# Kernel tuning notes

Hardware: AMD Instinct MI355X
Metric: run time of the kernel (lower is better)

Reference implementation:

```python
import jax, jax.numpy as jnp
import numpy as np
import math
from jax import lax


def quick_gelu(v):
    return v * jax.nn.sigmoid(1.702 * v)


def setup_inputs() -> dict:
    key = jax.random.key(0)
    k0, k1, k2, k3 = jax.random.split(key, 4)
    B, N, C, dim = 64, 1024, 768, 8
    x = jax.random.normal(k0, (B, N, C), dtype=jnp.float32)
    # adapter_down: Linear(C -> dim), xavier-ish init
    Wd = jax.random.normal(k1, (C, dim), dtype=jnp.float32) * (1.0 / math.sqrt(C))
    bd = jnp.zeros((dim,), dtype=jnp.float32)
    # adapter_conv: Conv2d(dim, dim, 3, stride=1, pad=1), HWIO layout
    Wc = jax.random.normal(k2, (3, 3, dim, dim), dtype=jnp.float32) * (1.0 / math.sqrt(9 * dim))
    bc = jnp.zeros((dim,), dtype=jnp.float32)
    # adapter_up: Linear(dim -> C); torch inits this to zeros, but use small
    # random values so the output/gradients are non-trivial for testing.
    Wu = jax.random.normal(k3, (dim, C), dtype=jnp.float32) * 0.02
    bu = jnp.zeros((C,), dtype=jnp.float32)
    return {"x": x, "Wd": Wd, "bd": bd, "Wc": Wc, "bc": bc, "Wu": Wu, "bu": bu}


def reference(x, Wd, bd, Wc, bc, Wu, bu):
    B, N, C = x.shape
    H = int(math.isqrt(N))  # N is a static perfect square (patch grid)
    dim = Wd.shape[1]
    # down projection: [B, N, C] -> [B, N, dim]
    x_down = jnp.einsum("bnc,cd->bnd", x, Wd) + bd
    # reshape to NHWC patch grid, activate, 3x3 same-pad conv
    x_patch = quick_gelu(x_down.reshape(B, H, H, dim))
    x_patch = lax.conv_general_dilated(
        x_patch, Wc, window_strides=(1, 1), padding="SAME",
        dimension_numbers=("NHWC", "HWIO", "NHWC")) + bc
    # flatten back, activate (dropout = identity in eval), up projection
    x_down = quick_gelu(x_patch.reshape(B, N, dim))
    x_up = jnp.einsum("bnd,dc->bnc", x_down, Wu) + bu
    return x_up
```

## Files before the change

kernel.cpp:

```cpp
#include <hip/hip_runtime.h>

#define B_  64
#define N_  1024
#define H_  32
#define C_  768
#define D_  8

__device__ __forceinline__ float qgelu(float v) {
    return v / (1.0f + __expf(-1.702f * v));
}

typedef float f32x4_t __attribute__((ext_vector_type(4)));
__device__ __forceinline__ float4 ntload4(const float4* p) {
    f32x4_t v = __builtin_nontemporal_load((const f32x4_t*)p);
    return make_float4(v.x, v.y, v.z, v.w);
}
__device__ __forceinline__ void ntstore4(float4 v, float4* p) {
    f32x4_t t; t.x = v.x; t.y = v.y; t.z = v.z; t.w = v.w;
    __builtin_nontemporal_store(t, (f32x4_t*)p);
}

__device__ __forceinline__ void reduce8(float* acc, int lane) {
    {
        const bool hi = lane & 1;
#pragma unroll
        for (int j = 0; j < 4; ++j) {
            const float a = acc[j], b = acc[j + 4];
            acc[j] = hi ? b : a;
            acc[j + 4] = hi ? a : b;
        }
#pragma unroll
        for (int j = 0; j < 4; ++j)
            acc[j] += __shfl_xor(acc[j + 4], 1, 64);
    }
    {
        const bool hi = lane & 2;
#pragma unroll
        for (int j = 0; j < 2; ++j) {
            const float a = acc[j], b = acc[j + 2];
            acc[j] = hi ? b : a;
            acc[j + 2] = hi ? a : b;
        }
#pragma unroll
        for (int j = 0; j < 2; ++j)
            acc[j] += __shfl_xor(acc[j + 2], 2, 64);
    }
    {
        const bool hi = lane & 4;
        const float a = acc[0], b = acc[1];
        acc[0] = hi ? b : a;
        acc[1] = hi ? a : b;
        acc[0] += __shfl_xor(acc[1], 4, 64);
    }
    acc[0] += __shfl_xor(acc[0], 8, 64);
    acc[0] += __shfl_xor(acc[0], 16, 64);
    acc[0] += __shfl_xor(acc[0], 32, 64);
}

__global__ __launch_bounds__(256) void k_down(
    const float* __restrict__ x, const float* __restrict__ Wd,
    const float* __restrict__ bd, float* __restrict__ t1)
{
    __shared__ float sW[D_ * C_];
    for (int i = threadIdx.x; i < D_ * C_; i += 256) {
        const int c = i >> 3, d = i & 7;
        sW[d * C_ + c] = Wd[i];
    }
    __syncthreads();

    const int wid  = threadIdx.x >> 6;
    const int lane = threadIdx.x & 63;
    const int dl   = 4 * (lane & 1) + 2 * ((lane >> 1) & 1) + ((lane >> 2) & 1);
    const float bias = bd[dl];

    const int gw = blockIdx.x * 4 + wid;

#pragma unroll 1
    for (int i = 0; i < 4; ++i) {
        const int p = gw * 4 + i;
        const float4* x0 = (const float4*)(x + (size_t)(2 * p) * C_);
        const float4* x1 = x0 + (C_ / 4);

        float4 va[3], vb[3];
#pragma unroll
        for (int k = 0; k < 3; ++k) {
            va[k] = ntload4(&x0[k * 64 + lane]);
            vb[k] = ntload4(&x1[k * 64 + lane]);
        }

        float a0[D_], a1[D_];
#pragma unroll
        for (int d = 0; d < D_; ++d) { a0[d] = 0.0f; a1[d] = 0.0f; }

#pragma unroll
        for (int k = 0; k < 3; ++k) {
#pragma unroll
            for (int d = 0; d < D_; ++d) {
                const float4 wv = *(const float4*)&sW[d * C_ + (k * 64 + lane) * 4];
                a0[d] += va[k].x * wv.x + va[k].y * wv.y
                       + va[k].z * wv.z + va[k].w * wv.w;
                a1[d] += vb[k].x * wv.x + vb[k].y * wv.y
                       + vb[k].z * wv.z + vb[k].w * wv.w;
            }
        }

        reduce8(a0, lane);
        reduce8(a1, lane);

        if (lane < 16) {
            const float s = (lane & 8) ? a1[0] : a0[0];
            t1[(size_t)(2 * p + ((lane >> 3) & 1)) * D_ + dl] = qgelu(s + bias);
        }
    }
}

__global__ __launch_bounds__(256, 4) void k_conv(
    const float* __restrict__ t1, const float* __restrict__ Wc,
    const float* __restrict__ bc, float* __restrict__ t2)
{
    __shared__ float sIn[10 * H_ * D_];
    __shared__ float sWc[9 * D_ * D_];
    __shared__ float sbc[D_];

    const int img   = blockIdx.x >> 2;
    const int strip = blockIdx.x & 3;
    const int h0    = strip * 8;
    const float* in = t1 + (size_t)img * N_ * D_;

#pragma unroll
    for (int j = 0; j < 10; ++j) {
        const int i  = threadIdx.x + j * 256;
        const int lr = i >> 8;
        const int rem = i & 255;
        const int g  = h0 - 1 + lr;
        sIn[i] = (g >= 0 && g < H_) ? in[(size_t)g * H_ * D_ + rem] : 0.0f;
    }
    for (int i = threadIdx.x; i < 9 * D_ * D_; i += 256) sWc[i] = Wc[i];
    if (threadIdx.x < D_) sbc[threadIdx.x] = bc[threadIdx.x];
    __syncthreads();

    const int lh = threadIdx.x >> 5;
    const int w  = threadIdx.x & 31;
    float acc[D_];
#pragma unroll
    for (int co = 0; co < D_; ++co) acc[co] = sbc[co];

#pragma unroll
    for (int kh = 0; kh < 3; ++kh) {
        const int lrow = lh + kh;
#pragma unroll
        for (int kw = 0; kw < 3; ++kw) {
            const int ww = w + kw - 1;
            if (ww < 0 || ww >= H_) continue;
            const float* ip = &sIn[(lrow * H_ + ww) * D_];
            const float* wp = &sWc[(kh * 3 + kw) * D_ * D_];
#pragma unroll
            for (int ci = 0; ci < D_; ++ci) {
                const float iv = ip[ci];
#pragma unroll
                for (int co = 0; co < D_; ++co)
                    acc[co] += iv * wp[ci * D_ + co];
            }
        }
    }
    float4 o0, o1;
    o0.x = qgelu(acc[0]); o0.y = qgelu(acc[1]);
    o0.z = qgelu(acc[2]); o0.w = qgelu(acc[3]);
    o1.x = qgelu(acc[4]); o1.y = qgelu(acc[5]);
    o1.z = qgelu(acc[6]); o1.w = qgelu(acc[7]);
    float* tp = t2 + ((size_t)img * N_ + (size_t)(h0 + lh) * H_ + w) * D_;
    *(float4*)tp       = o0;
    *(float4*)(tp + 4) = o1;
}

__global__ __launch_bounds__(256, 3) void k_up(
    const float* __restrict__ t2, const float* __restrict__ Wu,
    const float* __restrict__ bu, float* __restrict__ out, int nrows)
{
    const int wid  = threadIdx.x >> 6;
    const int lane = threadIdx.x & 63;

    float4 w[3][D_];
    float4 bias[3];
#pragma unroll
    for (int j = 0; j < 3; ++j) {
        bias[j] = *(const float4*)&bu[(lane + j * 64) * 4];
#pragma unroll
        for (int d = 0; d < D_; ++d)
            w[j][d] = *(const float4*)&Wu[d * C_ + (lane + j * 64) * 4];
    }

    const int stride = gridDim.x * 4;
    for (int row = blockIdx.x * 4 + wid; row < nrows; row += stride) {
        const float4* rp = (const float4*)(t2 + (size_t)row * D_);
        const float4 ra = rp[0];
        const float4 rb = rp[1];
        const float rv[D_] = { ra.x, ra.y, ra.z, ra.w, rb.x, rb.y, rb.z, rb.w };

#pragma unroll
        for (int j = 0; j < 3; ++j) {
            float4 o = bias[j];
#pragma unroll
            for (int d = 0; d < D_; ++d) {
                o.x += rv[d] * w[j][d].x;
                o.y += rv[d] * w[j][d].y;
                o.z += rv[d] * w[j][d].z;
                o.w += rv[d] * w[j][d].w;
            }
            ntstore4(o, (float4*)&out[(size_t)row * C_ + (size_t)(lane + j * 64) * 4]);
        }
    }
}

extern "C" void kernel_launch(void* const* d_in, const int* in_sizes, int n_in,
                              void* d_out, int out_size, void* d_ws, size_t ws_size,
                              hipStream_t stream) {
    const float* x  = (const float*)d_in[0];
    const float* Wd = (const float*)d_in[1];
    const float* bd = (const float*)d_in[2];
    const float* Wc = (const float*)d_in[3];
    const float* bc = (const float*)d_in[4];
    const float* Wu = (const float*)d_in[5];
    const float* bu = (const float*)d_in[6];
    float* out = (float*)d_out;

    const int nrows = B_ * N_;
    float* t1 = (float*)d_ws;
    float* t2 = t1 + (size_t)nrows * D_;

    k_down<<<2048, 256, 0, stream>>>(x, Wd, bd, t1);
    k_conv<<<B_ * 4, 256, 0, stream>>>(t1, Wc, bc, t2);
    k_up<<<768, 256, 0, stream>>>(t2, Wu, bu, out, nrows);
}
```

Measured before the change: 102.2 us.

## Fuse conv and up-projection and pipeline down/up stages across batch chunks

Merges the three kernels into one multi-role kernel launched five times over four batch chunks. Each launch runs the down projection for chunk s alongside the fused conv+up projection for chunk s-1, so the read-heavy and write-heavy phases overlap. The conv output now stays in shared memory instead of going through a global t2 buffer. In exchange there are more launches, the up stage gets less parallelism (64 blocks per chunk, each writing 256 rows), and the Wu registers held per thread may lower occupancy.

```diff
diff --git a/kernel.cpp b/kernel.cpp
--- a/kernel.cpp
+++ b/kernel.cpp
@@ -5,6 +5,12 @@
 #define H_  32
 #define C_  768
 #define D_  8
+
+#define QCHUNKS   4
+#define IMG_PER_Q (B_ / QCHUNKS)
+#define ROWS_PER_Q (IMG_PER_Q * N_)
+#define NDOWN     512
+#define NUP       (IMG_PER_Q * 4)
 
 __device__ __forceinline__ float qgelu(float v) {
     return v / (1.0f + __expf(-1.702f * v));
@@ -57,157 +63,153 @@
     acc[0] += __shfl_xor(acc[0], 32, 64);
 }
 
-__global__ __launch_bounds__(256) void k_down(
-    const float* __restrict__ x, const float* __restrict__ Wd,
-    const float* __restrict__ bd, float* __restrict__ t1)
+__global__ __launch_bounds__(256) void k_step(
+    const float* __restrict__ x,  const float* __restrict__ Wd,
+    const float* __restrict__ bd, float* __restrict__ t1,
+    const float* __restrict__ Wc, const float* __restrict__ bc,
+    const float* __restrict__ Wu, const float* __restrict__ bu,
+    float* __restrict__ out, int downBase, int nDown, int upImg0)
 {
-    __shared__ float sW[D_ * C_];
-    for (int i = threadIdx.x; i < D_ * C_; i += 256) {
-        const int c = i >> 3, d = i & 7;
-        sW[d * C_ + c] = Wd[i];
-    }
-    __syncthreads();
+    __shared__ float smem[D_ * C_];
 
     const int wid  = threadIdx.x >> 6;
     const int lane = threadIdx.x & 63;
-    const int dl   = 4 * (lane & 1) + 2 * ((lane >> 1) & 1) + ((lane >> 2) & 1);
-    const float bias = bd[dl];
-
-    const int gw = blockIdx.x * 4 + wid;
+
+    if ((int)blockIdx.x < nDown) {
+        float* sW = smem;
+        for (int i = threadIdx.x; i < D_ * C_; i += 256) {
+            const int c = i >> 3, d = i & 7;
+            sW[d * C_ + c] = Wd[i];
+        }
+        __syncthreads();
+
+        const int dl = 4 * (lane & 1) + 2 * ((lane >> 1) & 1) + ((lane >> 2) & 1);
+        const float bias = bd[dl];
+        const int pairBase = (downBase >> 1) + blockIdx.x * 16 + wid * 4;
 
 #pragma unroll 1
-    for (int i = 0; i < 4; ++i) {
-        const int p = gw * 4 + i;
-        const float4* x0 = (const float4*)(x + (size_t)(2 * p) * C_);
-        const float4* x1 = x0 + (C_ / 4);
-
-        float4 va[3], vb[3];
-#pragma unroll
-        for (int k = 0; k < 3; ++k) {
-            va[k] = ntload4(&x0[k * 64 + lane]);
-            vb[k] = ntload4(&x1[k * 64 + lane]);
-        }
-
-        float a0[D_], a1[D_];
-#pragma unroll
-        for (int d = 0; d < D_; ++d) { a0[d] = 0.0f; a1[d] = 0.0f; }
-
-#pragma unroll
-        for (int k = 0; k < 3; ++k) {
-#pragma unroll
-            for (int d = 0; d < D_; ++d) {
-                const float4 wv = *(const float4*)&sW[d * C_ + (k * 64 + lane) * 4];
-                a0[d] += va[k].x * wv.x + va[k].y * wv.y
-                       + va[k].z * wv.z + va[k].w * wv.w;
-                a1[d] += vb[k].x * wv.x + vb[k].y * wv.y
-                       + vb[k].z * wv.z + vb[k].w * wv.w;
-            }
-        }
-
-        reduce8(a0, lane);
-        reduce8(a1, lane);
-
-        if (lane < 16) {
-            const float s = (lane & 8) ? a1[0] : a0[0];
-            t1[(size_t)(2 * p + ((lane >> 3) & 1)) * D_ + dl] = qgelu(s + bias);
-        }
-    }
-}
-
-__global__ __launch_bounds__(256, 4) void k_conv(
-    const float* __restrict__ t1, const float* __restrict__ Wc,
-    const float* __restrict__ bc, float* __restrict__ t2)
-{
-    __shared__ float sIn[10 * H_ * D_];
-    __shared__ float sWc[9 * D_ * D_];
-    __shared__ float sbc[D_];
-
-    const int img   = blockIdx.x >> 2;
-    const int strip = blockIdx.x & 3;
-    const int h0    = strip * 8;
-    const float* in = t1 + (size_t)img * N_ * D_;
-
-#pragma unroll
-    for (int j = 0; j < 10; ++j) {
-        const int i  = threadIdx.x + j * 256;
-        const int lr = i >> 8;
-        const int rem = i & 255;
-        const int g  = h0 - 1 + lr;
-        sIn[i] = (g >= 0 && g < H_) ? in[(size_t)g * H_ * D_ + rem] : 0.0f;
-    }
-    for (int i = threadIdx.x; i < 9 * D_ * D_; i += 256) sWc[i] = Wc[i];
-    if (threadIdx.x < D_) sbc[threadIdx.x] = bc[threadIdx.x];
-    __syncthreads();
-
-    const int lh = threadIdx.x >> 5;
-    const int w  = threadIdx.x & 31;
-    float acc[D_];
-#pragma unroll
-    for (int co = 0; co < D_; ++co) acc[co] = sbc[co];
-
-#pragma unroll
-    for (int kh = 0; kh < 3; ++kh) {
-        const int lrow = lh + kh;
-#pragma unroll
-        for (int kw = 0; kw < 3; ++kw) {
-            const int ww = w + kw - 1;
-            if (ww < 0 || ww >= H_) continue;
-            const float* ip = &sIn[(lrow * H_ + ww) * D_];
-            const float* wp = &sWc[(kh * 3 + kw) * D_ * D_];
-#pragma unroll
-            for (int ci = 0; ci < D_; ++ci) {
-                const float iv = ip[ci];
-#pragma unroll
-                for (int co = 0; co < D_; ++co)
-                    acc[co] += iv * wp[ci * D_ + co];
-            }
-        }
-    }
-    float4 o0, o1;
-    o0.x = qgelu(acc[0]); o0.y = qgelu(acc[1]);
-    o0.z = qgelu(acc[2]); o0.w = qgelu(acc[3]);
-    o1.x = qgelu(acc[4]); o1.y = qgelu(acc[5]);
-    o1.z = qgelu(acc[6]); o1.w = qgelu(acc[7]);
-    float* tp = t2 + ((size_t)img * N_ + (size_t)(h0 + lh) * H_ + w) * D_;
-    *(float4*)tp       = o0;
-    *(float4*)(tp + 4) = o1;
-}
-
-__global__ __launch_bounds__(256, 3) void k_up(
-    const float* __restrict__ t2, const float* __restrict__ Wu,
-    const float* __restrict__ bu, float* __restrict__ out, int nrows)
-{
-    const int wid  = threadIdx.x >> 6;
-    const int lane = threadIdx.x & 63;
-
-    float4 w[3][D_];
-    float4 bias[3];
-#pragma unroll
-    for (int j = 0; j < 3; ++j) {
-        bias[j] = *(const float4*)&bu[(lane + j * 64) * 4];
-#pragma unroll
-        for (int d = 0; d < D_; ++d)
-            w[j][d] = *(const float4*)&Wu[d * C_ + (lane + j * 64) * 4];
-    }
-
-    const int stride = gridDim.x * 4;
-    for (int row = blockIdx.x * 4 + wid; row < nrows; row += stride) {
-        const float4* rp = (const float4*)(t2 + (size_t)row * D_);
-        const float4 ra = rp[0];
-        const float4 rb = rp[1];
-        const float rv[D_] = { ra.x, ra.y, ra.z, ra.w, rb.x, rb.y, rb.z, rb.w };
-
+        for (int i = 0; i < 4; ++i) {
+            const int p = pairBase + i;
+            const float4* x0 = (const float4*)(x + (size_t)(2 * p) * C_);
+            const float4* x1 = x0 + (C_ / 4);
+
+            float4 va[3], vb[3];
+#pragma unroll
+            for (int k = 0; k < 3; ++k) {
+                va[k] = ntload4(&x0[k * 64 + lane]);
+                vb[k] = ntload4(&x1[k * 64 + lane]);
+            }
+
+            float a0[D_], a1[D_];
+#pragma unroll
+            for (int d = 0; d < D_; ++d) { a0[d] = 0.0f; a1[d] = 0.0f; }
+
+#pragma unroll
+            for (int k = 0; k < 3; ++k) {
+#pragma unroll
+                for (int d = 0; d < D_; ++d) {
+                    const float4 wv = *(const float4*)&sW[d * C_ + (k * 64 + lane) * 4];
+                    a0[d] += va[k].x * wv.x + va[k].y * wv.y
+                           + va[k].z * wv.z + va[k].w * wv.w;
+                    a1[d] += vb[k].x * wv.x + vb[k].y * wv.y
+                           + vb[k].z * wv.z + vb[k].w * wv.w;
+                }
+            }
+
+            reduce8(a0, lane);
+            reduce8(a1, lane);
+
+            if (lane < 16) {
+                const float s = (lane & 8) ? a1[0] : a0[0];
+                t1[(size_t)(2 * p + ((lane >> 3) & 1)) * D_ + dl] = qgelu(s + bias);
+            }
+        }
+    } else {
+        float* sIn = smem;
+        float* sT2 = smem + 2560;
+        float* sWc = smem + 4608;
+        float* sbc = smem + 5184;
+
+        const int idx   = blockIdx.x - nDown;
+        const int img   = upImg0 + (idx >> 2);
+        const int strip = idx & 3;
+        const int h0    = strip * 8;
+        const float* in = t1 + (size_t)img * N_ * D_;
+
+#pragma unroll
+        for (int j = 0; j < 10; ++j) {
+            const int i   = threadIdx.x + j * 256;
+            const int lr  = i >> 8;
+            const int rem = i & 255;
+            const int g   = h0 - 1 + lr;
+            sIn[i] = (g >= 0 && g < H_) ? in[(size_t)g * H_ * D_ + rem] : 0.0f;
+        }
+        for (int i = threadIdx.x; i < 9 * D_ * D_; i += 256) sWc[i] = Wc[i];
+        if (threadIdx.x < D_) sbc[threadIdx.x] = bc[threadIdx.x];
+
+        float4 wu[3][D_];
+        float4 ub[3];
 #pragma unroll
         for (int j = 0; j < 3; ++j) {
-            float4 o = bias[j];
-#pragma unroll
-            for (int d = 0; d < D_; ++d) {
-                o.x += rv[d] * w[j][d].x;
-                o.y += rv[d] * w[j][d].y;
-                o.z += rv[d] * w[j][d].z;
-                o.w += rv[d] * w[j][d].w;
-            }
-            ntstore4(o, (float4*)&out[(size_t)row * C_ + (size_t)(lane + j * 64) * 4]);
+            ub[j] = *(const float4*)&bu[(lane + j * 64) * 4];
+#pragma unroll
+            for (int d = 0; d < D_; ++d)
+                wu[j][d] = *(const float4*)&Wu[d * C_ + (lane + j * 64) * 4];
+        }
+        __syncthreads();
+
+        {
+            const int lh = threadIdx.x >> 5;
+            const int w  = threadIdx.x & 31;
+            float acc[D_];
+#pragma unroll
+            for (int co = 0; co < D_; ++co) acc[co] = sbc[co];
+#pragma unroll
+            for (int kh = 0; kh < 3; ++kh) {
+                const int lrow = lh + kh;
+#pragma unroll
+                for (int kw = 0; kw < 3; ++kw) {
+                    const int ww = w + kw - 1;
+                    if (ww < 0 || ww >= H_) continue;
+                    const float* ip = &sIn[(lrow * H_ + ww) * D_];
+                    const float* wp = &sWc[(kh * 3 + kw) * D_ * D_];
+#pragma unroll
+                    for (int ci = 0; ci < D_; ++ci) {
+                        const float iv = ip[ci];
+#pragma unroll
+                        for (int co = 0; co < D_; ++co)
+                            acc[co] += iv * wp[ci * D_ + co];
+                    }
+                }
+            }
+            float* tp = &sT2[(lh * H_ + w) * D_];
+#pragma unroll
+            for (int co = 0; co < D_; ++co) tp[co] = qgelu(acc[co]);
+        }
+        __syncthreads();
+
+        const size_t rowBase = (size_t)img * N_ + strip * 256;
+#pragma unroll 1
+        for (int r = 0; r < 64; ++r) {
+            const int  row = wid * 64 + r;
+            const float* tv = &sT2[row * D_];
+            float rv[D_];
+#pragma unroll
+            for (int d = 0; d < D_; ++d) rv[d] = tv[d];
+
+            float* orow = out + (rowBase + row) * C_;
+#pragma unroll
+            for (int j = 0; j < 3; ++j) {
+                float4 o = ub[j];
+#pragma unroll
+                for (int d = 0; d < D_; ++d) {
+                    o.x += rv[d] * wu[j][d].x;
+                    o.y += rv[d] * wu[j][d].y;
+                    o.z += rv[d] * wu[j][d].z;
+                    o.w += rv[d] * wu[j][d].w;
+                }
+                ntstore4(o, (float4*)&orow[(lane + j * 64) * 4]);
+            }
         }
     }
 }
@@ -224,11 +226,15 @@
     const float* bu = (const float*)d_in[6];
     float* out = (float*)d_out;
 
-    const int nrows = B_ * N_;
     float* t1 = (float*)d_ws;
-    float* t2 = t1 + (size_t)nrows * D_;
-
-    k_down<<<2048, 256, 0, stream>>>(x, Wd, bd, t1);
-    k_conv<<<B_ * 4, 256, 0, stream>>>(t1, Wc, bc, t2);
-    k_up<<<768, 256, 0, stream>>>(t2, Wu, bu, out, nrows);
-}
+
+    for (int s = 0; s <= QCHUNKS; ++s) {
+        const int nDown  = (s < QCHUNKS) ? NDOWN : 0;
+        const int nUp    = (s > 0) ? NUP : 0;
+        const int grid   = nDown + nUp;
+        const int dBase  = s * ROWS_PER_Q;
+        const int uImg0  = (s - 1) * IMG_PER_Q;
+        k_step<<<grid, 256, 0, stream>>>(x, Wd, bd, t1, Wc, bc, Wu, bu, out,
+                                         dBase, nDown, uImg0);
+    }
+}
```

Measured after the change: 108.5 us. 6.2% more time.
